# Optimization experiments

Hardware: AMD Instinct MI355X
Metric: run time of the kernel (lower is better)

The kernel has to match this reference:

```python
import jax, jax.numpy as jnp
import numpy as np

B, M, H, D, K, V = 32, 4096, 32, 4096, 128, 128

def setup_inputs() -> dict:
    key = jax.random.key(0)
    ks = jax.random.split(key, 7)
    s = lambda fan: 1.0 / np.sqrt(fan)
    return {
        "x": jax.random.normal(ks[0], (B, D), jnp.float32),
        "K_prev": jax.random.normal(ks[1], (B, M, K), jnp.float32),
        "V_prev": jax.random.normal(ks[2], (B, M, V), jnp.float32),
        "P_q": jax.random.normal(ks[3], (H, D, K), jnp.float32) * s(D),
        "P_k": jax.random.normal(ks[4], (D, K), jnp.float32) * s(D),
        "P_v": jax.random.normal(ks[5], (D, V), jnp.float32) * s(D),
        "P_o": jax.random.normal(ks[6], (H, D, V), jnp.float32) * s(D),
    }

def reference(x, K_prev, V_prev, P_q, P_k, P_v, P_o):
    # per-head query projection: [b,d] x [h,d,k] -> [b,h,k]
    q = jnp.einsum('bd,hdk->bhk', x, P_q)
    # shared (multi-query) K/V projection of the new token, appended to cache
    k_new = jnp.einsum('bd,dk->bk', x, P_k)          # [b,k]
    v_new = jnp.einsum('bd,dv->bv', x, P_v)          # [b,v]
    K_new = jnp.concatenate([K_prev, k_new[:, None, :]], axis=1)  # [b,m+1,k]
    V_new = jnp.concatenate([V_prev, v_new[:, None, :]], axis=1)  # [b,m+1,v]
    # attention over shared cache
    logits = jnp.einsum('bhk,bmk->bhm', q, K_new)    # [b,h,m+1]
    w = jax.nn.softmax(logits, axis=-1)
    o = jnp.einsum('bhm,bmv->bhv', w, V_new)         # [b,h,v]
    y = jnp.einsum('bhv,hdv->bd', o, P_o)            # [b,d]
    return (y, K_new, V_new)
```

## Files before the change

### kernel.cpp

```cpp
#include <hip/hip_runtime.h>

#define B_ 32
#define M_ 4096
#define M1_ 4097
#define H_ 32
#define D_ 4096

typedef float float4_ __attribute__((ext_vector_type(4)));
typedef float f32x4 __attribute__((ext_vector_type(4)));
typedef short short8 __attribute__((ext_vector_type(8)));
typedef short short4_ __attribute__((ext_vector_type(4)));

#define KOFF 131072
#define VOFF 16912384

#define Q_OFF     0u
#define O_OFF     139264u
#define YPART_OFF 270336u
#define QPART_OFF 1318912u
#define APO_OFF   1318912u
#define MSUM_OFF  5513216u

__device__ __forceinline__ unsigned short f2bf(float f) {
  union { float f; unsigned u; } cv; cv.f = f;
  return (unsigned short)((cv.u + 0x7FFFu + ((cv.u >> 16) & 1u)) >> 16);
}
__device__ __forceinline__ float bf2f(unsigned short b) {
  union { unsigned u; float f; } cv; cv.u = ((unsigned)b) << 16;
  return cv.f;
}
__device__ __forceinline__ short8 pack8(const float* t) {
  short8 r;
#pragma unroll
  for (int j = 0; j < 8; ++j) r[j] = (short)f2bf(t[j]);
  return r;
}
__device__ __forceinline__ short8 load8cvt(const float* __restrict__ p) {
  float t[8];
  float4_ v0 = *(const float4_*)p;
  float4_ v1 = *(const float4_*)(p + 4);
#pragma unroll
  for (int j = 0; j < 4; ++j) { t[j] = v0[j]; t[4 + j] = v1[j]; }
  return pack8(t);
}

__global__ __launch_bounds__(256) void k_proj(const float* __restrict__ x,
    const float* __restrict__ Pq, const float* __restrict__ Pk,
    const float* __restrict__ Pv, float* __restrict__ qpart)
{
  int bid = blockIdx.x;
  int hh = bid >> 4;
  int c  = bid & 15;
  const float* W = (hh < 32) ? (Pq + (size_t)hh * D_ * 128)
                             : ((hh == 32) ? Pk : Pv);
  int d0 = c * 256;
  int tid = threadIdx.x;
  int w = tid >> 6, l = tid & 63, l15 = l & 15, lg = l >> 4;
  f32x4 acc[2][2] = {};
  for (int ks = 0; ks < 8; ++ks) {
    int dk = d0 + ks * 32 + lg * 8;
    short8 af[2];
#pragma unroll
    for (int bt = 0; bt < 2; ++bt)
      af[bt] = load8cvt(x + (size_t)(bt * 16 + l15) * D_ + dk);
    short8 bf[2];
#pragma unroll
    for (int nti = 0; nti < 2; ++nti) {
      int col = (2 * w + nti) * 16 + l15;
      float t[8];
#pragma unroll
      for (int j = 0; j < 8; ++j) t[j] = W[(size_t)(dk + j) * 128 + col];
      bf[nti] = pack8(t);
    }
#pragma unroll
    for (int bt = 0; bt < 2; ++bt)
#pragma unroll
      for (int nti = 0; nti < 2; ++nti)
        acc[bt][nti] = __builtin_amdgcn_mfma_f32_16x16x32_bf16(af[bt], bf[nti], acc[bt][nti], 0, 0, 0);
  }
#pragma unroll
  for (int bt = 0; bt < 2; ++bt)
#pragma unroll
    for (int nti = 0; nti < 2; ++nti) {
      int k = (2 * w + nti) * 16 + l15;
#pragma unroll
      for (int i = 0; i < 4; ++i) {
        int b = bt * 16 + lg * 4 + i;
        qpart[(size_t)((c * 34 + hh) * 32 + b) * 128 + k] = acc[bt][nti][i];
      }
    }
}

__global__ __launch_bounds__(256) void k_reduce_q(const float* __restrict__ qpart,
    float* __restrict__ q, float* __restrict__ dout)
{
  int idx = blockIdx.x * 256 + threadIdx.x;
  if (idx >= 34 * 32 * 128) return;
  float s = 0.f;
#pragma unroll
  for (int cc = 0; cc < 16; ++cc) s += qpart[(size_t)cc * 139264 + idx];
  q[idx] = s;
  int hh = idx >> 12;
  if (hh >= 32) {
    int b = (idx >> 7) & 31, k = idx & 127;
    size_t off = (hh == 32) ? (size_t)KOFF : (size_t)VOFF;
    dout[off + ((size_t)b * M1_ + M_) * 128 + k] = s;
  }
}

__global__ __launch_bounds__(256, 4) void k_attn(const float* __restrict__ Kp,
    const float* __restrict__ Vp, const float* __restrict__ q,
    float* __restrict__ dout, unsigned short* __restrict__ apo,
    float* __restrict__ msum)
{
  __shared__ unsigned short Vl[64][128];
  __shared__ float S[32][73];
  __shared__ unsigned short P[32][64];
  __shared__ float smax[32], ssum[32], sextra[32];
  int bid = blockIdx.x;
  int b = bid >> 6, c = bid & 63;
  int m0 = c * 64;
  int tid = threadIdx.x, w = tid >> 6, l = tid & 63, l15 = l & 15, lg = l >> 4;
  const float* Kt = Kp + ((size_t)b * M_ + m0) * 128;
  const float* Vt = Vp + ((size_t)b * M_ + m0) * 128;
  float* Kn = dout + KOFF + ((size_t)b * M1_ + m0) * 128;
  float* Vn = dout + VOFF + ((size_t)b * M1_ + m0) * 128;

  const float* Krow = Kt + (size_t)(w * 16 + l15) * 128;
  float4_ kr[8], vr[8];
#pragma unroll
  for (int ks = 0; ks < 4; ++ks) {
    kr[2 * ks]     = *(const float4_*)(Krow + ks * 32 + lg * 8);
    kr[2 * ks + 1] = *(const float4_*)(Krow + ks * 32 + lg * 8 + 4);
  }
#pragma unroll
  for (int i = 0; i < 8; ++i) vr[i] = ((const float4_*)Vt)[tid + i * 256];
  __builtin_amdgcn_sched_barrier(0);

  float* Knrow = Kn + (size_t)(w * 16 + l15) * 128;
#pragma unroll
  for (int ks = 0; ks < 4; ++ks) {
    *(float4_*)(Knrow + ks * 32 + lg * 8)     = kr[2 * ks];
    *(float4_*)(Knrow + ks * 32 + lg * 8 + 4) = kr[2 * ks + 1];
  }
#pragma unroll
  for (int i = 0; i < 8; ++i) {
    int idx = tid + i * 256;
    ((float4_*)Vn)[idx] = vr[i];
    int m = idx >> 5, v = (idx & 31) * 4;
    short4_ s;
#pragma unroll
    for (int j = 0; j < 4; ++j) s[j] = (short)f2bf(vr[i][j]);
    *(short4_*)&Vl[m][v] = s;
  }
  short8 kf[4];
#pragma unroll
  for (int ks = 0; ks < 4; ++ks) {
    float t[8];
#pragma unroll
    for (int j = 0; j < 4; ++j) { t[j] = kr[2 * ks][j]; t[4 + j] = kr[2 * ks + 1][j]; }
    kf[ks] = pack8(t);
  }

  f32x4 sacc[2] = {};
#pragma unroll
  for (int ks = 0; ks < 4; ++ks) {
#pragma unroll
    for (int ht = 0; ht < 2; ++ht) {
      short8 af = load8cvt(q + (size_t)((ht * 16 + l15) * 32 + b) * 128 + ks * 32 + lg * 8);
      sacc[ht] = __builtin_amdgcn_mfma_f32_16x16x32_bf16(af, kf[ks], sacc[ht], 0, 0, 0);
    }
  }
#pragma unroll
  for (int ht = 0; ht < 2; ++ht)
#pragma unroll
    for (int i = 0; i < 4; ++i)
      S[ht * 16 + lg * 4 + i][w * 16 + l15] = sacc[ht][i];

  if (c == 63 && tid < 32) {
    int h = tid;
    const float* qh = q + (size_t)(h * 32 + b) * 128;
    const float* kn = q + (size_t)(32 * 32 + b) * 128;
    float s = 0.f;
    for (int k = 0; k < 128; ++k) s += qh[k] * kn[k];
    S[h][64] = s;
  }
  __syncthreads();

  {
    int h = tid >> 3, i = tid & 7;
    float vals[8];
    float mx = -3e38f;
#pragma unroll
    for (int j = 0; j < 8; ++j) { vals[j] = S[h][i * 8 + j]; mx = fmaxf(mx, vals[j]); }
#pragma unroll
    for (int d = 1; d < 8; d <<= 1) mx = fmaxf(mx, __shfl_xor(mx, d));
    if (c == 63) mx = fmaxf(mx, S[h][64]);
    float se = 0.f;
    short8 pw;
#pragma unroll
    for (int j = 0; j < 8; ++j) {
      float p = __expf(vals[j] - mx);
      se += p;
      pw[j] = (short)f2bf(p);
    }
    *(short8*)((char*)P + h * 128 + ((i * 16) ^ ((h & 7) << 4))) = pw;
    if (c == 63 && i == 0) { float pe = __expf(S[h][64] - mx); se += pe; sextra[h] = pe; }
#pragma unroll
    for (int d = 1; d < 8; d <<= 1) se += __shfl_xor(se, d);
    if (i == 0) { smax[h] = mx; ssum[h] = se; }
  }
  __syncthreads();

  f32x4 oacc[2][2] = {};
#pragma unroll
  for (int ksv = 0; ksv < 2; ++ksv) {
    short8 af[2];
#pragma unroll
    for (int ht = 0; ht < 2; ++ht) {
      int h = ht * 16 + l15;
      af[ht] = *(const short8*)((const char*)P + h * 128 + ((ksv * 64 + lg * 16) ^ ((h & 7) << 4)));
    }
    short8 bf[2];
#pragma unroll
    for (int vti = 0; vti < 2; ++vti) {
      int v = w * 32 + vti * 16 + l15;
      short8 t;
#pragma unroll
      for (int j = 0; j < 8; ++j) t[j] = (short)Vl[ksv * 32 + lg * 8 + j][v];
      bf[vti] = t;
    }
#pragma unroll
    for (int ht = 0; ht < 2; ++ht)
#pragma unroll
      for (int vti = 0; vti < 2; ++vti)
        oacc[ht][vti] = __builtin_amdgcn_mfma_f32_16x16x32_bf16(af[ht], bf[vti], oacc[ht][vti], 0, 0, 0);
  }

  const float* vnew = q + (size_t)(33 * 32 + b) * 128;
#pragma unroll
  for (int ht = 0; ht < 2; ++ht)
#pragma unroll
    for (int vti = 0; vti < 2; ++vti) {
      int v = w * 32 + vti * 16 + l15;
#pragma unroll
      for (int i = 0; i < 4; ++i) {
        int h = ht * 16 + lg * 4 + i;
        float val = oacc[ht][vti][i];
        if (c == 63) val += sextra[h] * vnew[v];
        apo[((size_t)(b * 64 + c) * 32 + h) * 128 + v] = f2bf(val);
      }
    }
  if (tid < 32) {
    size_t base = ((size_t)(b * 64 + c) * 32 + tid) * 2;
    msum[base]     = smax[tid];
    msum[base + 1] = ssum[tid];
  }
}

__global__ __launch_bounds__(256) void k_combine(const unsigned short* __restrict__ apo,
    const float* __restrict__ msum, float* __restrict__ o)
{
  __shared__ float redN[4][128];
  __shared__ float redD[4];
  int bid = blockIdx.x;
  int b = bid >> 5, h = bid & 31;
  int tid = threadIdx.x, w = tid >> 6, l = tid & 63;

  float gm = msum[((size_t)(b * 64 + l) * 32 + h) * 2];
#pragma unroll
  for (int d = 1; d < 64; d <<= 1) gm = fmaxf(gm, __shfl_xor(gm, d));

  float num0 = 0.f, num1 = 0.f, den = 0.f;
#pragma unroll 4
  for (int i = 0; i < 16; ++i) {
    int cc = w * 16 + i;
    size_t slot = (size_t)(b * 64 + cc) * 32 + h;
    float sc = __expf(msum[slot * 2] - gm);
    den += sc * msum[slot * 2 + 1];
    unsigned pp = *(const unsigned*)&apo[slot * 128 + l * 2];
    num0 += sc * bf2f((unsigned short)(pp & 0xFFFFu));
    num1 += sc * bf2f((unsigned short)(pp >> 16));
  }
  redN[w][l * 2] = num0;
  redN[w][l * 2 + 1] = num1;
  if (l == 0) redD[w] = den;
  __syncthreads();
  if (tid < 128) {
    float num = redN[0][tid] + redN[1][tid] + redN[2][tid] + redN[3][tid];
    float dd  = redD[0] + redD[1] + redD[2] + redD[3];
    o[((size_t)(b * 32 + h)) * 128 + tid] = num / dd;
  }
}

__global__ __launch_bounds__(256) void k_out(const float* __restrict__ o,
    const float* __restrict__ Po, float* __restrict__ ypart)
{
  int bid = blockIdx.x;
  int dt = bid >> 3, hg = bid & 7;
  int tid = threadIdx.x, w = tid >> 6, l = tid & 63, l15 = l & 15, lg = l >> 4;
  int d = dt * 64 + w * 16 + l15;
  f32x4 acc[2] = {};
  for (int hi = 0; hi < 4; ++hi) {
    int h = hg * 4 + hi;
#pragma unroll
    for (int ks = 0; ks < 4; ++ks) {
      short8 af[2];
#pragma unroll
      for (int bt = 0; bt < 2; ++bt)
        af[bt] = load8cvt(o + ((size_t)((bt * 16 + l15) * 32 + h)) * 128 + ks * 32 + lg * 8);
      short8 bf = load8cvt(Po + ((size_t)h * D_ + d) * 128 + ks * 32 + lg * 8);
#pragma unroll
      for (int bt = 0; bt < 2; ++bt)
        acc[bt] = __builtin_amdgcn_mfma_f32_16x16x32_bf16(af[bt], bf, acc[bt], 0, 0, 0);
    }
  }
#pragma unroll
  for (int bt = 0; bt < 2; ++bt)
#pragma unroll
    for (int i = 0; i < 4; ++i) {
      int b = bt * 16 + lg * 4 + i;
      ypart[((size_t)(hg * 32 + b)) * 4096 + d] = acc[bt][i];
    }
}

__global__ __launch_bounds__(256) void k_reduce_y(const float* __restrict__ ypart,
    float* __restrict__ dout)
{
  int idx = blockIdx.x * 256 + threadIdx.x;
  float s = 0.f;
#pragma unroll
  for (int g = 0; g < 8; ++g) s += ypart[(size_t)g * 131072 + idx];
  dout[idx] = s;
}

extern "C" void kernel_launch(void* const* d_in, const int* in_sizes, int n_in,
                              void* d_out, int out_size, void* d_ws, size_t ws_size,
                              hipStream_t stream) {
  (void)in_sizes; (void)n_in; (void)out_size; (void)ws_size;
  const float* x  = (const float*)d_in[0];
  const float* Kp = (const float*)d_in[1];
  const float* Vp = (const float*)d_in[2];
  const float* Pq = (const float*)d_in[3];
  const float* Pk = (const float*)d_in[4];
  const float* Pv = (const float*)d_in[5];
  const float* Po = (const float*)d_in[6];
  float* out = (float*)d_out;
  float* ws  = (float*)d_ws;
  float* q     = ws + Q_OFF;
  float* o     = ws + O_OFF;
  float* ypart = ws + YPART_OFF;
  float* qpart = ws + QPART_OFF;
  unsigned short* apo = (unsigned short*)(ws + APO_OFF);
  float* msum  = ws + MSUM_OFF;

  hipLaunchKernelGGL(k_proj,     dim3(544),  dim3(256), 0, stream, x, Pq, Pk, Pv, qpart);
  hipLaunchKernelGGL(k_reduce_q, dim3(544),  dim3(256), 0, stream, qpart, q, out);
  hipLaunchKernelGGL(k_attn,     dim3(2048), dim3(256), 0, stream, Kp, Vp, q, out, apo, msum);
  hipLaunchKernelGGL(k_combine,  dim3(1024), dim3(256), 0, stream, apo, msum, o);
  hipLaunchKernelGGL(k_out,      dim3(512),  dim3(256), 0, stream, o, Po, ypart);
  hipLaunchKernelGGL(k_reduce_y, dim3(512),  dim3(256), 0, stream, ypart, out);
}
```

Measured before the change: 137.8 us.

## Load V tile directly into LDS via global_load_lds and hoist Q fragment loads

The V tile is now fetched with asynchronous global-to-LDS loads into an fp32 shared buffer instead of going through registers. The copy to the output cache and the bf16 conversion are deferred until after the QK^T stage, and the Q fragments are loaded up front before the MFMAs. This is meant to cut register pressure and overlap the V load latency with the score computation. In exchange, LDS use doubles (fp32 V tile) and launch bounds drop occupancy from 4 to 3 blocks per CU. The bf16 conversion also now happens on every LDS read of V.

```diff
diff --git a/kernel.cpp b/kernel.cpp
--- a/kernel.cpp
+++ b/kernel.cpp
@@ -42,6 +42,11 @@
 #pragma unroll
   for (int j = 0; j < 4; ++j) { t[j] = v0[j]; t[4 + j] = v1[j]; }
   return pack8(t);
+}
+__device__ __forceinline__ void load_lds16(const float* g, float* l) {
+  __builtin_amdgcn_global_load_lds(
+      (const __attribute__((address_space(1))) unsigned int*)g,
+      (__attribute__((address_space(3))) unsigned int*)l, 16, 0, 0);
 }
 
 __global__ __launch_bounds__(256) void k_proj(const float* __restrict__ x,
@@ -108,12 +113,12 @@
   }
 }
 
-__global__ __launch_bounds__(256, 4) void k_attn(const float* __restrict__ Kp,
+__global__ __launch_bounds__(256, 3) void k_attn(const float* __restrict__ Kp,
     const float* __restrict__ Vp, const float* __restrict__ q,
     float* __restrict__ dout, unsigned short* __restrict__ apo,
     float* __restrict__ msum)
 {
-  __shared__ unsigned short Vl[64][128];
+  __shared__ float Vf[64][128];
   __shared__ float S[32][73];
   __shared__ unsigned short P[32][64];
   __shared__ float smax[32], ssum[32], sextra[32];
@@ -127,14 +132,15 @@
   float* Vn = dout + VOFF + ((size_t)b * M1_ + m0) * 128;
 
   const float* Krow = Kt + (size_t)(w * 16 + l15) * 128;
-  float4_ kr[8], vr[8];
+  float4_ kr[8];
 #pragma unroll
   for (int ks = 0; ks < 4; ++ks) {
     kr[2 * ks]     = *(const float4_*)(Krow + ks * 32 + lg * 8);
     kr[2 * ks + 1] = *(const float4_*)(Krow + ks * 32 + lg * 8 + 4);
   }
 #pragma unroll
-  for (int i = 0; i < 8; ++i) vr[i] = ((const float4_*)Vt)[tid + i * 256];
+  for (int i = 0; i < 8; ++i)
+    load_lds16(Vt + (size_t)(i * 256 + tid) * 4, &Vf[0][0] + (i * 256 + w * 64) * 4);
   __builtin_amdgcn_sched_barrier(0);
 
   float* Knrow = Kn + (size_t)(w * 16 + l15) * 128;
@@ -143,16 +149,6 @@
     *(float4_*)(Knrow + ks * 32 + lg * 8)     = kr[2 * ks];
     *(float4_*)(Knrow + ks * 32 + lg * 8 + 4) = kr[2 * ks + 1];
   }
-#pragma unroll
-  for (int i = 0; i < 8; ++i) {
-    int idx = tid + i * 256;
-    ((float4_*)Vn)[idx] = vr[i];
-    int m = idx >> 5, v = (idx & 31) * 4;
-    short4_ s;
-#pragma unroll
-    for (int j = 0; j < 4; ++j) s[j] = (short)f2bf(vr[i][j]);
-    *(short4_*)&Vl[m][v] = s;
-  }
   short8 kf[4];
 #pragma unroll
   for (int ks = 0; ks < 4; ++ks) {
@@ -162,15 +158,18 @@
     kf[ks] = pack8(t);
   }
 
+  short8 af[2][4];
+#pragma unroll
+  for (int ks = 0; ks < 4; ++ks)
+#pragma unroll
+    for (int ht = 0; ht < 2; ++ht)
+      af[ht][ks] = load8cvt(q + (size_t)((ht * 16 + l15) * 32 + b) * 128 + ks * 32 + lg * 8);
   f32x4 sacc[2] = {};
 #pragma unroll
-  for (int ks = 0; ks < 4; ++ks) {
-#pragma unroll
-    for (int ht = 0; ht < 2; ++ht) {
-      short8 af = load8cvt(q + (size_t)((ht * 16 + l15) * 32 + b) * 128 + ks * 32 + lg * 8);
-      sacc[ht] = __builtin_amdgcn_mfma_f32_16x16x32_bf16(af, kf[ks], sacc[ht], 0, 0, 0);
-    }
-  }
+  for (int ks = 0; ks < 4; ++ks)
+#pragma unroll
+    for (int ht = 0; ht < 2; ++ht)
+      sacc[ht] = __builtin_amdgcn_mfma_f32_16x16x32_bf16(af[ht][ks], kf[ks], sacc[ht], 0, 0, 0);
 #pragma unroll
   for (int ht = 0; ht < 2; ++ht)
 #pragma unroll
@@ -187,6 +186,13 @@
   }
   __syncthreads();
 
+#pragma unroll
+  for (int i = 0; i < 8; ++i) {
+    int idx = tid + i * 256;
+    float4_ t = *(const float4_*)(&Vf[0][0] + idx * 4);
+    ((float4_*)Vn)[idx] = t;
+  }
+
   {
     int h = tid >> 3, i = tid & 7;
     float vals[8];
@@ -215,26 +221,26 @@
   f32x4 oacc[2][2] = {};
 #pragma unroll
   for (int ksv = 0; ksv < 2; ++ksv) {
-    short8 af[2];
+    short8 pa[2];
 #pragma unroll
     for (int ht = 0; ht < 2; ++ht) {
       int h = ht * 16 + l15;
-      af[ht] = *(const short8*)((const char*)P + h * 128 + ((ksv * 64 + lg * 16) ^ ((h & 7) << 4)));
+      pa[ht] = *(const short8*)((const char*)P + h * 128 + ((ksv * 64 + lg * 16) ^ ((h & 7) << 4)));
     }
     short8 bf[2];
 #pragma unroll
     for (int vti = 0; vti < 2; ++vti) {
       int v = w * 32 + vti * 16 + l15;
-      short8 t;
-#pragma unroll
-      for (int j = 0; j < 8; ++j) t[j] = (short)Vl[ksv * 32 + lg * 8 + j][v];
-      bf[vti] = t;
+      float t[8];
+#pragma unroll
+      for (int j = 0; j < 8; ++j) t[j] = Vf[ksv * 32 + lg * 8 + j][v];
+      bf[vti] = pack8(t);
     }
 #pragma unroll
     for (int ht = 0; ht < 2; ++ht)
 #pragma unroll
       for (int vti = 0; vti < 2; ++vti)
-        oacc[ht][vti] = __builtin_amdgcn_mfma_f32_16x16x32_bf16(af[ht], bf[vti], oacc[ht][vti], 0, 0, 0);
+        oacc[ht][vti] = __builtin_amdgcn_mfma_f32_16x16x32_bf16(pa[ht], bf[vti], oacc[ht][vti], 0, 0, 0);
   }
 
   const float* vnew = q + (size_t)(33 * 32 + b) * 128;
```

Result: faster. 134.5 us (-2.4%).
